# Optimization experiments

Measured on AMD Instinct MI355X. Metric: run time of the kernel, lower is better.

Reference implementation:

```python
import jax, jax.numpy as jnp
import numpy as np

B_, L, D_MODEL = 8, 2048, 512
EXPAND, D_STATE, HEADDIM, NGROUPS, D_CONV = 2, 16, 64, 1, 4
D_INNER = EXPAND * D_MODEL            # 1024
NHEADS = D_INNER // HEADDIM           # 16
CONV_DIM = D_INNER + 2 * NGROUPS * D_STATE   # 1056
D_IN_PROJ = 2 * D_INNER + 2 * NGROUPS * D_STATE + NHEADS  # 2096
EPS = 1e-5


def _mamba_params(key):
    ks = jax.random.split(key, 5)
    in_proj_w = jax.random.normal(ks[0], (D_IN_PROJ, D_MODEL), jnp.float32) * (D_MODEL ** -0.5)
    conv_w = jax.random.normal(ks[1], (CONV_DIM, 1, D_CONV), jnp.float32) * (D_CONV ** -0.5)
    conv_b = jnp.zeros((CONV_DIM,), jnp.float32)
    # inverse-softplus of dt ~ U[1e-3, 0.1] (mamba-ssm style init)
    dt_bias = jnp.log(jnp.expm1(jax.random.uniform(ks[2], (NHEADS,), jnp.float32, 1e-3, 0.1)))
    A_log = jnp.log(jax.random.uniform(ks[3], (NHEADS,), jnp.float32, 1.0, 16.0))
    Dp = jnp.ones((NHEADS,), jnp.float32)
    norm_w = jnp.ones((D_INNER,), jnp.float32)
    out_proj_w = jax.random.normal(ks[4], (D_MODEL, D_INNER), jnp.float32) * (D_INNER ** -0.5)
    return [in_proj_w, conv_w, conv_b, dt_bias, A_log, Dp, norm_w, out_proj_w]


def setup_inputs() -> dict:
    key = jax.random.key(0)
    k0, k1, k2 = jax.random.split(key, 3)
    d = {"x": jax.random.normal(k0, (B_, L, D_MODEL), jnp.float32)}
    names = ["in_proj_w", "conv_w", "conv_b", "dt_bias", "A_log", "Dp", "norm_w", "out_proj_w"]
    for pre, k in (("fwd_", k1), ("bwd_", k2)):
        for n, p in zip(names, _mamba_params(k)):
            d[pre + n] = p
    return d


def _silu(v):
    return v * jax.nn.sigmoid(v)


def _mamba2(u, in_proj_w, conv_w, conv_b, dt_bias, A_log, Dp, norm_w, out_proj_w):
    b, l, _ = u.shape
    zxbcdt = u @ in_proj_w.T                                # (b,l,D_IN_PROJ)
    z, xBC, dt = jnp.split(zxbcdt, [D_INNER, D_INNER + CONV_DIM], axis=-1)
    # causal depthwise conv1d + silu
    xc = jnp.transpose(xBC, (0, 2, 1))                      # (b,C,l)
    xc = jax.lax.conv_general_dilated(xc, conv_w, (1,), [(D_CONV - 1, 0)],
                                      feature_group_count=CONV_DIM)
    xBC = _silu(jnp.transpose(xc, (0, 2, 1)) + conv_b)      # (b,l,C)
    xs, Bm, Cm = jnp.split(xBC, [D_INNER, D_INNER + NGROUPS * D_STATE], axis=-1)
    xs = xs.reshape(b, l, NHEADS, HEADDIM)
    Bm = Bm.reshape(b, l, NGROUPS, D_STATE)[:, :, 0]        # ngroups=1 -> (b,l,N)
    Cm = Cm.reshape(b, l, NGROUPS, D_STATE)[:, :, 0]
    dt = jax.nn.softplus(dt + dt_bias)                      # (b,l,H)
    A = -jnp.exp(A_log)                                     # (H,)
    dA = jnp.exp(dt * A)                                    # (b,l,H), in (0,1)

    def step(h, inp):
        dA_t, dt_t, x_t, B_t, C_t = inp
        h = h * dA_t[:, :, None, None] + jnp.einsum('bh,bhp,bn->bhpn', dt_t, x_t, B_t)
        y = jnp.einsum('bhpn,bn->bhp', h, C_t)
        return h, y

    h0 = jnp.zeros((b, NHEADS, HEADDIM, D_STATE), u.dtype)
    seq = (jnp.moveaxis(dA, 1, 0), jnp.moveaxis(dt, 1, 0), jnp.moveaxis(xs, 1, 0),
           jnp.moveaxis(Bm, 1, 0), jnp.moveaxis(Cm, 1, 0))
    _, ys = jax.lax.scan(step, h0, seq)
    y = jnp.moveaxis(ys, 0, 1) + xs * Dp[None, None, :, None]   # (b,l,H,P)
    y = y.reshape(b, l, D_INNER)
    # RMSNormGated (norm_before_gate=False): rmsnorm(y * silu(z)) * w
    y = y * _silu(z)
    y = y * jax.lax.rsqrt(jnp.mean(y * y, axis=-1, keepdims=True) + EPS) * norm_w
    return y @ out_proj_w.T


def reference(x,
              fwd_in_proj_w, fwd_conv_w, fwd_conv_b, fwd_dt_bias, fwd_A_log, fwd_Dp, fwd_norm_w, fwd_out_proj_w,
              bwd_in_proj_w, bwd_conv_w, bwd_conv_b, bwd_dt_bias, bwd_A_log, bwd_Dp, bwd_norm_w, bwd_out_proj_w):
    fwd = _mamba2(x, fwd_in_proj_w, fwd_conv_w, fwd_conv_b, fwd_dt_bias, fwd_A_log, fwd_Dp, fwd_norm_w, fwd_out_proj_w)
    bwd = _mamba2(x[:, ::-1], bwd_in_proj_w, bwd_conv_w, bwd_conv_b, bwd_dt_bias, bwd_A_log, bwd_Dp, bwd_norm_w, bwd_out_proj_w)
    return fwd + bwd[:, ::-1]
```

## Files before the change

### kernel.cpp

```cpp
#include <hip/hip_runtime.h>
#include <stdint.h>

#define L_SEQ   2048
#define BATCH   8
#define DMODEL  512
#define DINNER  1024
#define NHEADS  16
#define HEADDIM 64
#define DSTATE  16
#define CONVDIM 1056
#define DINPROJ 2096
#define NPROJ   4192
#define NPROJ_P 4224
#define NROWS   (BATCH*L_SEQ)
#define NCH     16
#define CHLEN   128
#define XBCW    1072

typedef __attribute__((ext_vector_type(8))) short short8;
typedef __attribute__((ext_vector_type(4))) float f32x4;

static __device__ __forceinline__ unsigned short f2bf(float f) {
    unsigned int u = __float_as_uint(f);
    u += 0x7FFF + ((u >> 16) & 1);
    return (unsigned short)(u >> 16);
}
static __device__ __forceinline__ float bf2f(unsigned short u) {
    return __uint_as_float((unsigned int)u << 16);
}
static __device__ __forceinline__ float silu(float v) {
    return v / (1.f + __expf(-v));
}
static __device__ __forceinline__ void glds16(const unsigned short* g, unsigned short* l) {
    __builtin_amdgcn_global_load_lds(
        (const __attribute__((address_space(1))) unsigned int*)g,
        (__attribute__((address_space(3))) unsigned int*)l, 16, 0, 0);
}

__global__ void k_cvt(const float* __restrict__ src, unsigned short* __restrict__ dst, int n) {
    int i = blockIdx.x * 256 + threadIdx.x;
    if (i < n) dst[i] = f2bf(src[i]);
}

__global__ void k_build_w1(const float* __restrict__ fw, const float* __restrict__ bw,
                           unsigned short* __restrict__ dst) {
    int i = blockIdx.x * 256 + threadIdx.x;
    const int FS = DINPROJ * DMODEL;
    if (i < NPROJ_P * DMODEL)
        dst[i] = (i < 2 * FS) ? f2bf(i < FS ? fw[i] : bw[i - FS]) : 0;
}

__global__ void k_build_w2(const float* __restrict__ fw, const float* __restrict__ bw,
                           unsigned short* __restrict__ dst) {
    int i = blockIdx.x * 256 + threadIdx.x;
    if (i < 512 * 2048) {
        int n = i >> 11, k = i & 2047;
        float v = (k < DINNER) ? fw[n * DINNER + k] : bw[n * DINNER + k - DINNER];
        dst[i] = f2bf(v);
    }
}

#define BM 128
#define BN 128
#define BK 32

#define GEMM_BODY(EPILOGUE)                                                                 \
    __shared__ __align__(16) unsigned short as[BM][BK];                                     \
    __shared__ __align__(16) unsigned short bs[BN][BK];                                     \
    const int tid = threadIdx.x;                                                            \
    const int lane = tid & 63;                                                              \
    const int wave = tid >> 6;                                                              \
    const int wm = (wave & 1) * 64;                                                         \
    const int wn = (wave >> 1) * 64;                                                        \
    const int l16 = lane & 15;                                                              \
    const int q = lane >> 4;                                                                \
    const int sr = wave * 32;                                                               \
    const int lr = lane >> 2;                                                               \
    const int lc = (lane & 3) * 8;                                                          \
    f32x4 acc[4][4];                                                                        \
    for (int i = 0; i < 4; i++)                                                             \
        for (int j = 0; j < 4; j++) acc[i][j] = (f32x4){0.f, 0.f, 0.f, 0.f};                \
    const unsigned short* Ab = A + (size_t)(bm + sr + lr) * K + lc;                         \
    const unsigned short* Bb = Bw + (size_t)(bn + sr + lr) * K + lc;                        \
    for (int kb = 0; kb < K; kb += BK) {                                                    \
        glds16(Ab + kb, &as[sr][0]);                                                        \
        glds16(Ab + (size_t)16 * K + kb, &as[sr + 16][0]);                                  \
        glds16(Bb + kb, &bs[sr][0]);                                                        \
        glds16(Bb + (size_t)16 * K + kb, &bs[sr + 16][0]);                                  \
        __syncthreads();                                                                    \
        short8 af[4], bfr[4];                                                               \
        for (int i = 0; i < 4; i++) af[i] = *(const short8*)&as[wm + i * 16 + l16][q * 8];  \
        for (int j = 0; j < 4; j++) bfr[j] = *(const short8*)&bs[wn + j * 16 + l16][q * 8]; \
        for (int i = 0; i < 4; i++)                                                         \
            for (int j = 0; j < 4; j++)                                                     \
                acc[i][j] = __builtin_amdgcn_mfma_f32_16x16x32_bf16(af[i], bfr[j], acc[i][j], 0, 0, 0); \
        __syncthreads();                                                                    \
    }                                                                                       \
    EPILOGUE

__global__ __launch_bounds__(256) void k_gemm_proj(const unsigned short* __restrict__ A,
                                                   const unsigned short* __restrict__ Bw,
                                                   unsigned short* __restrict__ ZG,
                                                   unsigned short* __restrict__ XBCDT,
                                                   int M, int N, int K) {
    const int lin = blockIdx.x;
    const int xcd = lin & 7;
    const int idx = lin >> 3;
    const int mloc = idx & 15;
    const int n_tile = idx >> 4;
    const int bm = (mloc * 8 + xcd) * BM;
    const int bn = n_tile * BN;
    GEMM_BODY({
        for (int i = 0; i < 4; i++) {
            int row0 = bm + wm + i * 16 + q * 4;
            for (int j = 0; j < 4; j++) {
                int col = bn + wn + j * 16 + l16;
                if (col < N) {
                    int dir = col >= DINPROJ;
                    int cc = col - dir * DINPROJ;
                    for (int r = 0; r < 4; r++) {
                        unsigned short v = f2bf(acc[i][j][r]);
                        size_t rowo = (size_t)(dir * NROWS + row0 + r);
                        if (cc < DINNER)
                            ZG[rowo * DINNER + cc] = v;
                        else
                            XBCDT[rowo * XBCW + (cc - DINNER)] = v;
                    }
                }
            }
        }
    })
}

__global__ __launch_bounds__(256) void k_gemm_out(const unsigned short* __restrict__ A,
                                                  const unsigned short* __restrict__ Bw,
                                                  float* __restrict__ C,
                                                  int M, int N, int K) {
    const int lin = blockIdx.x;
    const int xcd = lin & 7;
    const int idx = lin >> 3;
    const int g = idx >> 4;
    const int rem = idx & 15;
    const int n_tile = rem >> 2;
    const int mloc = (g << 2) | (rem & 3);
    const int bm = (mloc * 8 + xcd) * BM;
    const int bn = n_tile * BN;
    GEMM_BODY({
        for (int i = 0; i < 4; i++) {
            int row0 = bm + wm + i * 16 + q * 4;
            for (int j = 0; j < 4; j++) {
                int col = bn + wn + j * 16 + l16;
                for (int r = 0; r < 4; r++)
                    C[(size_t)(row0 + r) * N + col] = acc[i][j][r];
            }
        }
    })
}

__global__ __launch_bounds__(256) void k_conv2(const unsigned short* __restrict__ XBCDT,
                                               const float* __restrict__ fw_w, const float* __restrict__ fw_b,
                                               const float* __restrict__ bw_w, const float* __restrict__ bw_b,
                                               unsigned short* __restrict__ XS, float* __restrict__ BCb) {
    __shared__ unsigned short sm[70][256];
    int t = threadIdx.x;
    int bidx = blockIdx.x;
    int lcn = bidx & 31;
    int b   = (bidx >> 5) & 7;
    int dir = (bidx >> 8) & 1;
    int ct  = bidx >> 9;
    int c0 = ct * 256;
    int l0 = lcn * 64;
    int c = c0 + t;
    const unsigned short* src = XBCDT + (size_t)dir * NROWS * XBCW;
    bool cok = (c < CONVDIM);
#pragma unroll 2
    for (int r = 0; r < 70; r++) {
        int li = l0 - 3 + r;
        unsigned short v = 0;
        if (li >= 0 && li < L_SEQ && cok)
            v = src[(size_t)((b << 11) + li) * XBCW + c];
        sm[r][t] = v;
    }
    __syncthreads();
    if (!cok) return;
    const float* w = (dir ? bw_w : fw_w) + c * 4;
    float bias = (dir ? bw_b : fw_b)[c];
    float wr[4];
    if (dir) { wr[0] = w[3]; wr[1] = w[2]; wr[2] = w[1]; wr[3] = w[0]; }
    else     { wr[0] = w[0]; wr[1] = w[1]; wr[2] = w[2]; wr[3] = w[3]; }
    int o = dir ? 3 : 0;
    float w0 = bf2f(sm[o][t]), w1 = bf2f(sm[o + 1][t]), w2 = bf2f(sm[o + 2][t]);
    unsigned short* xso = XS + (size_t)dir * NROWS * DINNER;
    float* bco = BCb + (size_t)dir * NROWS * 32;
    int rowbase = (b << 11) + l0;
#pragma unroll 4
    for (int l = 0; l < 64; l++) {
        float w3 = bf2f(sm[l + o + 3][t]);
        float acc = ((wr[0] * w0 + wr[1] * w1) + (wr[2] * w2 + wr[3] * w3)) + bias;
        float v = silu(acc);
        int row = rowbase + l;
        if (c < DINNER)
            xso[(size_t)row * DINNER + c] = f2bf(v);
        else
            bco[(size_t)row * 32 + (c - DINNER)] = v;
        w0 = w1; w1 = w2; w2 = w3;
    }
}

__global__ void k_dt(const unsigned short* __restrict__ XBCDT,
                     const float* __restrict__ fdtb, const float* __restrict__ fAl,
                     const float* __restrict__ bdtb, const float* __restrict__ bAl,
                     float* __restrict__ DT, float* __restrict__ DA) {
    int gid = blockIdx.x * 256 + threadIdx.x;
    if (gid >= 2 * NROWS * NHEADS) return;
    int h = gid & 15;
    int row = (gid >> 4) & (NROWS - 1);
    int dir = gid >> 18;
    float dtb = (dir ? bdtb : fdtb)[h];
    float Al = (dir ? bAl : fAl)[h];
    float x = bf2f(XBCDT[(size_t)(dir * NROWS + row) * XBCW + CONVDIM + h]) + dtb;
    float dt = (x > 15.f) ? x : log1pf(__expf(x));
    float dA = __expf(-__expf(Al) * dt);
    DT[gid] = dt;
    DA[gid] = dA;
}

__global__ __launch_bounds__(64) void k_scan_state(const unsigned short* __restrict__ XS,
                                                   const float* __restrict__ BCb,
                                                   const float* __restrict__ DT,
                                                   const float* __restrict__ DA,
                                                   float* __restrict__ S, float* __restrict__ P) {
    int idx = blockIdx.x;
    int c = idx & 15, h = (idx >> 4) & 15, b = (idx >> 8) & 7, dir = idx >> 11;
    int p = threadIdx.x;
    const unsigned short* xs = XS + (size_t)dir * NROWS * DINNER;
    const float* bc = BCb + (size_t)dir * NROWS * 32;
    const float* dtp = DT + (size_t)dir * NROWS * NHEADS;
    const float* dap = DA + (size_t)dir * NROWS * NHEADS;
    float hreg[16];
#pragma unroll
    for (int n = 0; n < 16; n++) hreg[n] = 0.f;
    float Pp = 1.f;
    for (int tl = 0; tl < CHLEN; ++tl) {
        int t = c * CHLEN + tl;
        int l = dir ? (L_SEQ - 1 - t) : t;
        int row = (b << 11) + l;
        float xv = bf2f(xs[(size_t)row * DINNER + h * HEADDIM + p]);
        float dt = dtp[row * 16 + h];
        float dA = dap[row * 16 + h];
        f32x4 Bv[4];
#pragma unroll
        for (int qq = 0; qq < 4; qq++) Bv[qq] = *(const f32x4*)&bc[(size_t)row * 32 + qq * 4];
        float kk = dt * xv;
#pragma unroll
        for (int n = 0; n < 16; n++) hreg[n] = fmaf(hreg[n], dA, kk * Bv[n >> 2][n & 3]);
        Pp *= dA;
    }
#pragma unroll
    for (int qq = 0; qq < 4; qq++) {
        f32x4 v = {hreg[qq * 4], hreg[qq * 4 + 1], hreg[qq * 4 + 2], hreg[qq * 4 + 3]};
        *(f32x4*)&S[(size_t)idx * 1024 + p * 16 + qq * 4] = v;
    }
    if (p == 0) P[idx] = Pp;
}

__global__ void k_combine(float* __restrict__ S, const float* __restrict__ P) {
    int gid = blockIdx.x * 256 + threadIdx.x;
    if (gid >= 2 * 8 * 16 * 1024) return;
    int pn = gid & 1023;
    int base = gid >> 10;
    float H = 0.f;
    for (int c = 0; c < NCH; c++) {
        size_t o = ((size_t)base * NCH + c) * 1024 + pn;
        float s = S[o];
        S[o] = H;
        H = H * P[base * NCH + c] + s;
    }
}

__global__ __launch_bounds__(64) void k_scan_out(const unsigned short* __restrict__ XS,
                                                 const float* __restrict__ BCb,
                                                 const float* __restrict__ DT,
                                                 const float* __restrict__ DA,
                                                 const float* __restrict__ Hinit,
                                                 const float* __restrict__ fDp,
                                                 const float* __restrict__ bDp,
                                                 unsigned short* __restrict__ Y) {
    int idx = blockIdx.x;
    int c = idx & 15, h = (idx >> 4) & 15, b = (idx >> 8) & 7, dir = idx >> 11;
    int p = threadIdx.x;
    const unsigned short* xs = XS + (size_t)dir * NROWS * DINNER;
    const float* bc = BCb + (size_t)dir * NROWS * 32;
    const float* dtp = DT + (size_t)dir * NROWS * NHEADS;
    const float* dap = DA + (size_t)dir * NROWS * NHEADS;
    unsigned short* yo = Y + (size_t)dir * NROWS * DINNER;
    float Dpv = (dir ? bDp : fDp)[h];
    float hreg[16];
#pragma unroll
    for (int qq = 0; qq < 4; qq++) {
        f32x4 v = *(const f32x4*)&Hinit[(size_t)idx * 1024 + p * 16 + qq * 4];
#pragma unroll
        for (int e = 0; e < 4; e++) hreg[qq * 4 + e] = v[e];
    }
    for (int tl = 0; tl < CHLEN; ++tl) {
        int t = c * CHLEN + tl;
        int l = dir ? (L_SEQ - 1 - t) : t;
        int row = (b << 11) + l;
        float xv = bf2f(xs[(size_t)row * DINNER + h * HEADDIM + p]);
        float dt = dtp[row * 16 + h];
        float dA = dap[row * 16 + h];
        f32x4 Bv[4], Cv[4];
#pragma unroll
        for (int qq = 0; qq < 4; qq++) Bv[qq] = *(const f32x4*)&bc[(size_t)row * 32 + qq * 4];
#pragma unroll
        for (int qq = 0; qq < 4; qq++) Cv[qq] = *(const f32x4*)&bc[(size_t)row * 32 + 16 + qq * 4];
        float kk = dt * xv;
        float y = 0.f;
#pragma unroll
        for (int n = 0; n < 16; n++) {
            hreg[n] = fmaf(hreg[n], dA, kk * Bv[n >> 2][n & 3]);
            y = fmaf(hreg[n], Cv[n >> 2][n & 3], y);
        }
        yo[(size_t)row * DINNER + h * HEADDIM + p] = f2bf(y + xv * Dpv);
    }
}

__global__ __launch_bounds__(256) void k_gatenorm(const unsigned short* __restrict__ Y,
                                                  const unsigned short* __restrict__ ZG,
                                                  const float* __restrict__ fnw,
                                                  const float* __restrict__ bnw,
                                                  unsigned short* __restrict__ NRM) {
    int bid = blockIdx.x;
    int dir = bid >> 14;
    int row = bid & (NROWS - 1);
    int tid = threadIdx.x;
    int c = tid * 4;
    ushort4 yu = *(const ushort4*)&Y[(size_t)(dir * NROWS + row) * DINNER + c];
    ushort4 zu = *(const ushort4*)&ZG[(size_t)(dir * NROWS + row) * DINNER + c];
    float v0 = bf2f(yu.x) * silu(bf2f(zu.x));
    float v1 = bf2f(yu.y) * silu(bf2f(zu.y));
    float v2 = bf2f(yu.z) * silu(bf2f(zu.z));
    float v3 = bf2f(yu.w) * silu(bf2f(zu.w));
    float ss = v0 * v0 + v1 * v1 + v2 * v2 + v3 * v3;
#pragma unroll
    for (int off = 32; off > 0; off >>= 1) ss += __shfl_down(ss, off);
    __shared__ float red[4];
    if ((tid & 63) == 0) red[tid >> 6] = ss;
    __syncthreads();
    float tot = red[0] + red[1] + red[2] + red[3];
    float scale = rsqrtf(tot * (1.f / 1024.f) + 1e-5f);
    const float* nw = dir ? bnw : fnw;
    ushort4 o;
    o.x = f2bf(v0 * scale * nw[c]);
    o.y = f2bf(v1 * scale * nw[c + 1]);
    o.z = f2bf(v2 * scale * nw[c + 2]);
    o.w = f2bf(v3 * scale * nw[c + 3]);
    *(ushort4*)&NRM[(size_t)row * 2048 + dir * DINNER + c] = o;
}

extern "C" void kernel_launch(void* const* d_in, const int* in_sizes, int n_in,
                              void* d_out, int out_size, void* d_ws, size_t ws_size,
                              hipStream_t stream) {
    const float* x     = (const float*)d_in[0];
    const float* f_inw = (const float*)d_in[1];
    const float* f_cw  = (const float*)d_in[2];
    const float* f_cb  = (const float*)d_in[3];
    const float* f_dtb = (const float*)d_in[4];
    const float* f_Al  = (const float*)d_in[5];
    const float* f_Dp  = (const float*)d_in[6];
    const float* f_nw  = (const float*)d_in[7];
    const float* f_ow  = (const float*)d_in[8];
    const float* b_inw = (const float*)d_in[9];
    const float* b_cw  = (const float*)d_in[10];
    const float* b_cb  = (const float*)d_in[11];
    const float* b_dtb = (const float*)d_in[12];
    const float* b_Al  = (const float*)d_in[13];
    const float* b_Dp  = (const float*)d_in[14];
    const float* b_nw  = (const float*)d_in[15];
    const float* b_ow  = (const float*)d_in[16];

    char* ws = (char*)d_ws;
    size_t off = 0;
    auto alloc = [&](size_t bytes) {
        void* p = ws + off;
        off += (bytes + 255) & ~(size_t)255;
        return p;
    };
    unsigned short* XBCDT = (unsigned short*)alloc((size_t)2 * NROWS * XBCW * 2);
    unsigned short* NRM   = XBCDT;
    unsigned short* XS    = (unsigned short*)alloc((size_t)2 * NROWS * DINNER * 2);
    unsigned short* Yb    = XS;
    unsigned short* ZG    = (unsigned short*)alloc((size_t)2 * NROWS * DINNER * 2);
    unsigned short* W2    = (unsigned short*)alloc((size_t)512 * 2048 * 2);
    float* BCb  = (float*)alloc((size_t)2 * NROWS * 32 * 4);
    float* DT   = (float*)alloc((size_t)2 * NROWS * NHEADS * 4);
    float* DA   = (float*)alloc((size_t)2 * NROWS * NHEADS * 4);
    char* unionBase = (char*)alloc((size_t)16777216 + (size_t)NPROJ_P * DMODEL * 2);
    unsigned short* XB = (unsigned short*)unionBase;
    unsigned short* W1 = (unsigned short*)(unionBase + 16777216);
    float* S = (float*)unionBase;
    float* P = (float*)(unionBase + 16777216);

    if (ws_size < off) return;

    {
        int n = NROWS * DMODEL;
        k_cvt<<<(n + 255) / 256, 256, 0, stream>>>(x, XB, n);
    }
    {
        int n = NPROJ_P * DMODEL;
        k_build_w1<<<(n + 255) / 256, 256, 0, stream>>>(f_inw, b_inw, W1);
    }
    {
        int n = 512 * 2048;
        k_build_w2<<<(n + 255) / 256, 256, 0, stream>>>(f_ow, b_ow, W2);
    }
    k_gemm_proj<<<8 * 16 * 33, 256, 0, stream>>>(XB, W1, ZG, XBCDT, NROWS, NPROJ, DMODEL);
    k_conv2<<<5 * 2 * 8 * 32, 256, 0, stream>>>(XBCDT, f_cw, f_cb, b_cw, b_cb, XS, BCb);
    {
        int n = 2 * NROWS * NHEADS;
        k_dt<<<(n + 255) / 256, 256, 0, stream>>>(XBCDT, f_dtb, f_Al, b_dtb, b_Al, DT, DA);
    }
    k_scan_state<<<2 * 8 * 16 * NCH, 64, 0, stream>>>(XS, BCb, DT, DA, S, P);
    {
        int n = 2 * 8 * 16 * 1024;
        k_combine<<<(n + 255) / 256, 256, 0, stream>>>(S, P);
    }
    k_scan_out<<<2 * 8 * 16 * NCH, 64, 0, stream>>>(XS, BCb, DT, DA, S, f_Dp, b_Dp, Yb);
    k_gatenorm<<<2 * NROWS, 256, 0, stream>>>(Yb, ZG, f_nw, b_nw, NRM);
    k_gemm_out<<<8 * 16 * 4, 256, 0, stream>>>(NRM, W2, (float*)d_out, NROWS, 512, 2048);
}
```

Baseline: 551.9 us.

## Double-buffer GEMM LDS loads, split-K output GEMM, fuse prep kernels, unroll scans

The GEMM mainloop now uses two LDS buffers so the next K-tile's global-to-LDS loads are issued before the current tile's MFMAs, which removes one barrier per iteration. The output GEMM is split in two along K to double its block count, with a new add kernel that sums the partial results. The partial buffer reuses the ZG workspace, which is no longer needed after gatenorm. The three conversion kernels are merged into one launch, and the scan loops get unroll pragmas. The split-K path adds an extra fp32 read-modify-write pass over the output.

Result: no change. 556.7 us (+0.9%).

```diff
diff --git a/kernel.cpp b/kernel.cpp
--- a/kernel.cpp
+++ b/kernel.cpp
@@ -37,26 +37,26 @@
         (__attribute__((address_space(3))) unsigned int*)l, 16, 0, 0);
 }
 
-__global__ void k_cvt(const float* __restrict__ src, unsigned short* __restrict__ dst, int n) {
+#define PREP_N1 (NROWS*DMODEL)
+#define PREP_N2 (NPROJ_P*DMODEL)
+#define PREP_N3 (512*2048)
+__global__ void k_prep(const float* __restrict__ x,
+                       const float* __restrict__ fwi, const float* __restrict__ bwi,
+                       const float* __restrict__ fow, const float* __restrict__ bow,
+                       unsigned short* __restrict__ XB, unsigned short* __restrict__ W1,
+                       unsigned short* __restrict__ W2) {
     int i = blockIdx.x * 256 + threadIdx.x;
-    if (i < n) dst[i] = f2bf(src[i]);
-}
-
-__global__ void k_build_w1(const float* __restrict__ fw, const float* __restrict__ bw,
-                           unsigned short* __restrict__ dst) {
-    int i = blockIdx.x * 256 + threadIdx.x;
-    const int FS = DINPROJ * DMODEL;
-    if (i < NPROJ_P * DMODEL)
-        dst[i] = (i < 2 * FS) ? f2bf(i < FS ? fw[i] : bw[i - FS]) : 0;
-}
-
-__global__ void k_build_w2(const float* __restrict__ fw, const float* __restrict__ bw,
-                           unsigned short* __restrict__ dst) {
-    int i = blockIdx.x * 256 + threadIdx.x;
-    if (i < 512 * 2048) {
-        int n = i >> 11, k = i & 2047;
-        float v = (k < DINNER) ? fw[n * DINNER + k] : bw[n * DINNER + k - DINNER];
-        dst[i] = f2bf(v);
+    if (i < PREP_N1) {
+        XB[i] = f2bf(x[i]);
+    } else if (i < PREP_N1 + PREP_N2) {
+        int j = i - PREP_N1;
+        const int FS = DINPROJ * DMODEL;
+        W1[j] = (j < 2 * FS) ? f2bf(j < FS ? fwi[j] : bwi[j - FS]) : 0;
+    } else if (i < PREP_N1 + PREP_N2 + PREP_N3) {
+        int j = i - PREP_N1 - PREP_N2;
+        int n = j >> 11, k = j & 2047;
+        float v = (k < DINNER) ? fow[n * DINNER + k] : bow[n * DINNER + k - DINNER];
+        W2[j] = f2bf(v);
     }
 }
 
@@ -64,9 +64,9 @@
 #define BN 128
 #define BK 32
 
-#define GEMM_BODY(EPILOGUE)                                                                 \
-    __shared__ __align__(16) unsigned short as[BM][BK];                                     \
-    __shared__ __align__(16) unsigned short bs[BN][BK];                                     \
+#define GEMM_BODY(NROUNDS, EPILOGUE)                                                        \
+    __shared__ __align__(16) unsigned short as[2][BM][BK];                                  \
+    __shared__ __align__(16) unsigned short bs[2][BN][BK];                                  \
     const int tid = threadIdx.x;                                                            \
     const int lane = tid & 63;                                                              \
     const int wave = tid >> 6;                                                              \
@@ -80,29 +80,38 @@
     f32x4 acc[4][4];                                                                        \
     for (int i = 0; i < 4; i++)                                                             \
         for (int j = 0; j < 4; j++) acc[i][j] = (f32x4){0.f, 0.f, 0.f, 0.f};                \
-    const unsigned short* Ab = A + (size_t)(bm + sr + lr) * K + lc;                         \
-    const unsigned short* Bb = Bw + (size_t)(bn + sr + lr) * K + lc;                        \
-    for (int kb = 0; kb < K; kb += BK) {                                                    \
-        glds16(Ab + kb, &as[sr][0]);                                                        \
-        glds16(Ab + (size_t)16 * K + kb, &as[sr + 16][0]);                                  \
-        glds16(Bb + kb, &bs[sr][0]);                                                        \
-        glds16(Bb + (size_t)16 * K + kb, &bs[sr + 16][0]);                                  \
-        __syncthreads();                                                                    \
+    const unsigned short* Ab = A + (size_t)(bm + sr + lr) * K + koff + lc;                  \
+    const unsigned short* Bb = Bw + (size_t)(bn + sr + lr) * K + koff + lc;                 \
+    glds16(Ab, &as[0][sr][0]);                                                              \
+    glds16(Ab + (size_t)16 * K, &as[0][sr + 16][0]);                                        \
+    glds16(Bb, &bs[0][sr][0]);                                                              \
+    glds16(Bb + (size_t)16 * K, &bs[0][sr + 16][0]);                                        \
+    __syncthreads();                                                                        \
+    for (int r = 0; r < NROUNDS; r++) {                                                     \
+        const int pb = r & 1;                                                               \
+        if (r + 1 < NROUNDS) {               \
+            const int kb = (r + 1) * BK;                                                    \
+            glds16(Ab + kb, &as[pb ^ 1][sr][0]);                                            \
+            glds16(Ab + (size_t)16 * K + kb, &as[pb ^ 1][sr + 16][0]);                      \
+            glds16(Bb + kb, &bs[pb ^ 1][sr][0]);                                            \
+            glds16(Bb + (size_t)16 * K + kb, &bs[pb ^ 1][sr + 16][0]);                      \
+        }                                                                                   \
         short8 af[4], bfr[4];                                                               \
-        for (int i = 0; i < 4; i++) af[i] = *(const short8*)&as[wm + i * 16 + l16][q * 8];  \
-        for (int j = 0; j < 4; j++) bfr[j] = *(const short8*)&bs[wn + j * 16 + l16][q * 8]; \
+        for (int i = 0; i < 4; i++) af[i] = *(const short8*)&as[pb][wm + i * 16 + l16][q * 8]; \
+        for (int j = 0; j < 4; j++) bfr[j] = *(const short8*)&bs[pb][wn + j * 16 + l16][q * 8]; \
         for (int i = 0; i < 4; i++)                                                         \
             for (int j = 0; j < 4; j++)                                                     \
                 acc[i][j] = __builtin_amdgcn_mfma_f32_16x16x32_bf16(af[i], bfr[j], acc[i][j], 0, 0, 0); \
-        __syncthreads();                                                                    \
+        __syncthreads();             \
     }                                                                                       \
     EPILOGUE
 
 __global__ __launch_bounds__(256) void k_gemm_proj(const unsigned short* __restrict__ A,
                                                    const unsigned short* __restrict__ Bw,
                                                    unsigned short* __restrict__ ZG,
-                                                   unsigned short* __restrict__ XBCDT,
-                                                   int M, int N, int K) {
+                                                   unsigned short* __restrict__ XBCDT) {
+    const int K = DMODEL;
+    const int N = NPROJ;
     const int lin = blockIdx.x;
     const int xcd = lin & 7;
     const int idx = lin >> 3;
@@ -110,7 +119,8 @@
     const int n_tile = idx >> 4;
     const int bm = (mloc * 8 + xcd) * BM;
     const int bn = n_tile * BN;
-    GEMM_BODY({
+    const int koff = 0;
+    GEMM_BODY(16, {
         for (int i = 0; i < 4; i++) {
             int row0 = bm + wm + i * 16 + q * 4;
             for (int j = 0; j < 4; j++) {
@@ -134,18 +144,24 @@
 
 __global__ __launch_bounds__(256) void k_gemm_out(const unsigned short* __restrict__ A,
                                                   const unsigned short* __restrict__ Bw,
-                                                  float* __restrict__ C,
-                                                  int M, int N, int K) {
+                                                  float* __restrict__ C0,
+                                                  float* __restrict__ C1) {
+    const int K = 2048;
+    const int N = 512;
     const int lin = blockIdx.x;
     const int xcd = lin & 7;
     const int idx = lin >> 3;
-    const int g = idx >> 4;
-    const int rem = idx & 15;
-    const int n_tile = rem >> 2;
-    const int mloc = (g << 2) | (rem & 3);
+    const int ksplit = idx >> 6;
+    const int rem = idx & 63;
+    const int g = rem >> 4;
+    const int r2 = rem & 15;
+    const int n_tile = r2 >> 2;
+    const int mloc = (g << 2) | (r2 & 3);
     const int bm = (mloc * 8 + xcd) * BM;
     const int bn = n_tile * BN;
-    GEMM_BODY({
+    const int koff = ksplit * 1024;
+    float* __restrict__ C = ksplit ? C1 : C0;
+    GEMM_BODY(32, {
         for (int i = 0; i < 4; i++) {
             int row0 = bm + wm + i * 16 + q * 4;
             for (int j = 0; j < 4; j++) {
@@ -155,6 +171,16 @@
             }
         }
     })
+}
+
+__global__ void k_addout(float* __restrict__ C0, const float* __restrict__ C1) {
+    int i = blockIdx.x * 256 + threadIdx.x;
+    if (i < NROWS * 512 / 4) {
+        f32x4 a = *(const f32x4*)&C0[i * 4];
+        f32x4 b = *(const f32x4*)&C1[i * 4];
+        a += b;
+        *(f32x4*)&C0[i * 4] = a;
+    }
 }
 
 __global__ __launch_bounds__(256) void k_conv2(const unsigned short* __restrict__ XBCDT,
@@ -241,6 +267,7 @@
 #pragma unroll
     for (int n = 0; n < 16; n++) hreg[n] = 0.f;
     float Pp = 1.f;
+#pragma unroll 4
     for (int tl = 0; tl < CHLEN; ++tl) {
         int t = c * CHLEN + tl;
         int l = dir ? (L_SEQ - 1 - t) : t;
@@ -270,6 +297,7 @@
     int pn = gid & 1023;
     int base = gid >> 10;
     float H = 0.f;
+#pragma unroll 4
     for (int c = 0; c < NCH; c++) {
         size_t o = ((size_t)base * NCH + c) * 1024 + pn;
         float s = S[o];
@@ -302,6 +330,7 @@
 #pragma unroll
         for (int e = 0; e < 4; e++) hreg[qq * 4 + e] = v[e];
     }
+#pragma unroll 4
     for (int tl = 0; tl < CHLEN; ++tl) {
         int t = c * CHLEN + tl;
         int l = dir ? (L_SEQ - 1 - t) : t;
@@ -391,6 +420,7 @@
     unsigned short* XS    = (unsigned short*)alloc((size_t)2 * NROWS * DINNER * 2);
     unsigned short* Yb    = XS;
     unsigned short* ZG    = (unsigned short*)alloc((size_t)2 * NROWS * DINNER * 2);
+    float* PBUF = (float*)ZG;
     unsigned short* W2    = (unsigned short*)alloc((size_t)512 * 2048 * 2);
     float* BCb  = (float*)alloc((size_t)2 * NROWS * 32 * 4);
     float* DT   = (float*)alloc((size_t)2 * NROWS * NHEADS * 4);
@@ -404,18 +434,10 @@
     if (ws_size < off) return;
 
     {
-        int n = NROWS * DMODEL;
-        k_cvt<<<(n + 255) / 256, 256, 0, stream>>>(x, XB, n);
-    }
-    {
-        int n = NPROJ_P * DMODEL;
-        k_build_w1<<<(n + 255) / 256, 256, 0, stream>>>(f_inw, b_inw, W1);
-    }
-    {
-        int n = 512 * 2048;
-        k_build_w2<<<(n + 255) / 256, 256, 0, stream>>>(f_ow, b_ow, W2);
-    }
-    k_gemm_proj<<<8 * 16 * 33, 256, 0, stream>>>(XB, W1, ZG, XBCDT, NROWS, NPROJ, DMODEL);
+        int n = PREP_N1 + PREP_N2 + PREP_N3;
+        k_prep<<<(n + 255) / 256, 256, 0, stream>>>(x, f_inw, b_inw, f_ow, b_ow, XB, W1, W2);
+    }
+    k_gemm_proj<<<8 * 16 * 33, 256, 0, stream>>>(XB, W1, ZG, XBCDT);
     k_conv2<<<5 * 2 * 8 * 32, 256, 0, stream>>>(XBCDT, f_cw, f_cb, b_cw, b_cb, XS, BCb);
     {
         int n = 2 * NROWS * NHEADS;
@@ -428,5 +450,9 @@
     }
     k_scan_out<<<2 * 8 * 16 * NCH, 64, 0, stream>>>(XS, BCb, DT, DA, S, f_Dp, b_Dp, Yb);
     k_gatenorm<<<2 * NROWS, 256, 0, stream>>>(Yb, ZG, f_nw, b_nw, NRM);
-    k_gemm_out<<<8 * 16 * 4, 256, 0, stream>>>(NRM, W2, (float*)d_out, NROWS, 512, 2048);
-}
+    k_gemm_out<<<8 * 128, 256, 0, stream>>>(NRM, W2, (float*)d_out, PBUF);
+    {
+        int n = NROWS * 512 / 4;
+        k_addout<<<(n + 255) / 256, 256, 0, stream>>>((float*)d_out, PBUF);
+    }
+}
```
